# Performance work log

Hardware: AMD Instinct MI355X
Metric: run time of the kernel (lower is better)

Reference implementation:

```python
import jax, jax.numpy as jnp
import numpy as np

RES = 32
SPATIAL = 3
NUM_VOCAB = 3
EMBED_DIM = 256
BATCH = 8
LAYER_SIZES = (8, 64, 512, 4096, 32768)   # full-octree token counts at depths 1..5
CONV_SIZE = {3: 4, 4: 8}                  # layer_idx -> conv kernel==stride (2**(sd-1), 2**sd)
PARAM_NAMES = ([f"val_emb_{l}" for l in range(5)] + [f"pos_emb_{l}" for l in range(5)]
               + [f"dep_emb_{l}" for l in range(3)]
               + ["conv_w_3", "conv_b_3", "conv_w_4", "conv_b_4"])


def _forward(value, depth, position, params):
    # depth layout is static per construction: tokens sorted by depth with LAYER_SIZES counts,
    # so the per-depth boolean masking of the torch code reduces to static slices.
    outs, start = [], 0
    for l, n in enumerate(LAYER_SIZES):
        v = value[:, start:start + n]          # [B, n]
        d = depth[:, start:start + n]          # [B, n]
        p = position[:, start:start + n]       # [B, n, SPATIAL]
        start += n
        pe = params[f"pos_emb_{l}"]            # [SPATIAL, 2*RES, E]
        x = (params[f"val_emb_{l}"][v]
             + pe[0][p[..., 0]] + pe[1][p[..., 1]] + pe[2][p[..., 2]])
        if l < 3:
            # BasicEmbeddingA: value + depth + spatial embeddings summed
            x = x + params[f"dep_emb_{l}"][d]
        else:
            # ConvolutionEmbeddingA: Conv1d(E, E, kernel=stride=k) shrinks seq by k.
            # stride==kernel -> expressible as a reshape + einsum contraction.
            k = CONV_SIZE[l]
            B, T, E = x.shape
            xr = x.reshape(B, T // k, k, E)
            x = jnp.einsum('btke,oek->bto', xr, params[f"conv_w_{l}"]) + params[f"conv_b_{l}"]
        outs.append(x)
    # all samples have identical per-depth lengths -> pad_sequence is a plain concat
    return jnp.concatenate(outs, axis=1)       # [B, 5704, E]


def setup_inputs() -> dict:
    keys = iter(jax.random.split(jax.random.key(0), 64))
    S = sum(LAYER_SIZES)
    value = jax.random.randint(next(keys), (BATCH, S), 1, NUM_VOCAB + 1, dtype=jnp.int32)
    depth = jnp.broadcast_to(
        jnp.concatenate([jnp.full((n,), l + 1, jnp.int32) for l, n in enumerate(LAYER_SIZES)]),
        (BATCH, S))
    position = jax.random.randint(next(keys), (BATCH, S, SPATIAL), 1, 2 * RES, dtype=jnp.int32)
    inp = {"value": value, "depth": depth, "position": position}

    def emb(k, n):  # padding_idx=0 -> zero row
        return (jax.random.normal(k, (n, EMBED_DIM)) * 0.02).at[0].set(0.0)

    for l in range(5):
        inp[f"val_emb_{l}"] = emb(next(keys), NUM_VOCAB + 1)
        inp[f"pos_emb_{l}"] = (jax.random.normal(next(keys), (SPATIAL, 2 * RES, EMBED_DIM)) * 0.02).at[:, 0].set(0.0)
    for l in range(3):
        inp[f"dep_emb_{l}"] = emb(next(keys), 6)
    for l in (3, 4):
        k = CONV_SIZE[l]
        inp[f"conv_w_{l}"] = jax.random.normal(next(keys), (EMBED_DIM, EMBED_DIM, k)) / np.float32(np.sqrt(EMBED_DIM * k))
        inp[f"conv_b_{l}"] = jnp.zeros((EMBED_DIM,), jnp.float32)
    return inp


def reference(value, depth, position,
              val_emb_0, val_emb_1, val_emb_2, val_emb_3, val_emb_4,
              pos_emb_0, pos_emb_1, pos_emb_2, pos_emb_3, pos_emb_4,
              dep_emb_0, dep_emb_1, dep_emb_2,
              conv_w_3, conv_b_3, conv_w_4, conv_b_4):
    params = dict(zip(PARAM_NAMES, (val_emb_0, val_emb_1, val_emb_2, val_emb_3, val_emb_4,
                                    pos_emb_0, pos_emb_1, pos_emb_2, pos_emb_3, pos_emb_4,
                                    dep_emb_0, dep_emb_1, dep_emb_2,
                                    conv_w_3, conv_b_3, conv_w_4, conv_b_4)))
    return _forward(value, depth, position, params)
```

## Files before the change

### kernel.cpp

```cpp
#include <hip/hip_runtime.h>

#define S_TOT 37448
#define OUT_T 5704
#define EMB 256
#define TROWS 384
#define TSZ (TROWS * 256)

typedef unsigned short u16;
typedef __bf16 bf16x8 __attribute__((ext_vector_type(8)));
typedef float f32x4 __attribute__((ext_vector_type(4)));
typedef float f32x2 __attribute__((ext_vector_type(2)));
typedef unsigned short u16x4 __attribute__((ext_vector_type(4)));
typedef unsigned short u16x8 __attribute__((ext_vector_type(8)));

__device__ __forceinline__ u16 f2bf(float f) {
  union { float f; unsigned int i; } v;
  v.f = f;
  unsigned int x = v.i;
  return (u16)((x + 0x7fffu + ((x >> 16) & 1u)) >> 16);
}
__device__ __forceinline__ f32x2 bfp(unsigned u) {
  union { unsigned u; float f; } lo, hi;
  lo.u = u << 16;
  hi.u = u & 0xffff0000u;
  return (f32x2){lo.f, hi.f};
}

#define GLOAD_LDS16(g, l)                                                     \
  __builtin_amdgcn_global_load_lds((const __attribute__((address_space(1))) void*)(g), \
                                   (__attribute__((address_space(3))) void*)(l), 16, 0, 0)

__global__ __launch_bounds__(256) void transpose_w(
    const float* __restrict__ w3, const float* __restrict__ w4,
    u16* __restrict__ wt3, u16* __restrict__ wt4) {
  const int i = blockIdx.x * 256 + threadIdx.x;
  if (i < 256 * 1024) {
    const int o = i >> 10, c = i & 1023, kk = c >> 8, e = c & 255;
    wt3[i] = f2bf(w3[o * 1024 + e * 4 + kk]);
  }
  if (i < 256 * 2048) {
    const int o = i >> 11, c = i & 2047, kk = c >> 8, e = c & 255;
    wt4[i] = f2bf(w4[o * 2048 + e * 8 + kk]);
  }
}

__global__ __launch_bounds__(512) void proj_tables(
    const float* __restrict__ ve3, const float* __restrict__ pe3, const u16* __restrict__ wt3,
    const float* __restrict__ ve4, const float* __restrict__ pe4, const u16* __restrict__ wt4,
    u16* __restrict__ Tm) {
  __shared__ __align__(16) u16 As[64 * 32];
  __shared__ __align__(16) u16 Bs[256 * 32];
  const int bid = blockIdx.x;
  const int p = bid / 6, rb = bid % 6;
  const float *ve, *pe;
  const u16* wt;
  int K, kk;
  if (p < 4) { ve = ve3; pe = pe3; wt = wt3; K = 1024; kk = p; }
  else       { ve = ve4; pe = pe4; wt = wt4; K = 2048; kk = p - 4; }
  u16* To = Tm + (long)p * TSZ;
  const int tid = threadIdx.x;
  const int lane = tid & 63, wid = tid >> 6;
  const int wr = wid >> 2, wc = wid & 3;
  const int fr = lane & 15, fq = lane >> 4;
  const int row0 = rb * 64;

  const int arow = tid >> 3, acg = tid & 7;
  const int agran = acg >> 1, ahalf = acg & 1;
  const int aoff = arow * 32 + (agran ^ ((arow >> 1) & 3)) * 8 + ahalf * 4;
  const int gr = row0 + arow;
  const bool two = (gr < 256);
  const float* s1 = two ? (ve + (gr >> 6) * 256) : (pe + (gr - 192) * 256);
  const float* s2 = two ? (pe + (gr & 63) * 256) : nullptr;

  f32x4 acc[2][4];
#pragma unroll
  for (int m = 0; m < 2; ++m)
#pragma unroll
    for (int n = 0; n < 4; ++n) acc[m][n] = (f32x4){0.f, 0.f, 0.f, 0.f};

  for (int s = 0; s < 8; ++s) {
    {
      float4 x = *(const float4*)(s1 + s * 32 + acg * 4);
      if (two) {
        const float4 y = *(const float4*)(s2 + s * 32 + acg * 4);
        x.x += y.x; x.y += y.y; x.z += y.z; x.w += y.w;
      }
      u16x4 pk;
      pk[0] = f2bf(x.x); pk[1] = f2bf(x.y); pk[2] = f2bf(x.z); pk[3] = f2bf(x.w);
      *(u16x4*)(&As[aoff]) = pk;
    }
#pragma unroll
    for (int j = 0; j < 2; ++j) {
      const int rl = j * 128 + wid * 16 + (lane >> 2);
      const int gc = (lane & 3) ^ ((rl >> 1) & 3);
      const u16* src = wt + (long)rl * K + (kk * 8 + s) * 32 + gc * 8;
      u16* dst = &Bs[(j * 128 + wid * 16) * 32];
      GLOAD_LDS16(src, dst);
    }
    __syncthreads();
    bf16x8 af[2], bfv[4];
#pragma unroll
    for (int m = 0; m < 2; ++m) {
      const int r = wr * 32 + m * 16 + fr;
      u16x8 t = *(const u16x8*)(&As[r * 32 + (fq ^ ((r >> 1) & 3)) * 8]);
      af[m] = __builtin_bit_cast(bf16x8, t);
    }
#pragma unroll
    for (int n = 0; n < 4; ++n) {
      const int o = wc * 64 + n * 16 + fr;
      u16x8 t = *(const u16x8*)(&Bs[o * 32 + (fq ^ ((o >> 1) & 3)) * 8]);
      bfv[n] = __builtin_bit_cast(bf16x8, t);
    }
#pragma unroll
    for (int m = 0; m < 2; ++m)
#pragma unroll
      for (int n = 0; n < 4; ++n)
        acc[m][n] = __builtin_amdgcn_mfma_f32_16x16x32_bf16(af[m], bfv[n], acc[m][n], 0, 0, 0);
    __syncthreads();
  }
#pragma unroll
  for (int m = 0; m < 2; ++m)
#pragma unroll
    for (int reg = 0; reg < 4; ++reg) {
      const int r = row0 + wr * 32 + m * 16 + fq * 4 + reg;
#pragma unroll
      for (int n = 0; n < 4; ++n)
        To[r * 256 + wc * 64 + n * 16 + fr] = f2bf(acc[m][n][reg]);
    }
}

template <int CK, int LOG2T, int S0, int OUT0>
__device__ __forceinline__ void rowpair_gather(
    int pair, int lane, const int* __restrict__ value,
    const int* __restrict__ position, const u16* __restrict__ Tp,
    const float4& bz0, const float4& bz1, float* __restrict__ out) {
  constexpr int T = 1 << LOG2T;
  const int row = pair * 2 + (lane >> 5);
  const int l32 = lane & 31;
  const int b = row >> LOG2T, to = row & (T - 1);
  const long base = (long)b * S_TOT + S0 + to * CK;
  int vv[CK];
  *(int4*)vv = *(const int4*)(value + base);
  if constexpr (CK == 8) *(int4*)(vv + 4) = *(const int4*)(value + base + 4);
  int pp[3 * CK];
#pragma unroll
  for (int j = 0; j < 3 * CK / 2; ++j)
    *(int2*)(pp + 2 * j) = *(const int2*)(position + base * 3 + 2 * j);

  const int o0 = l32 * 8;
  f32x2 ac0 = (f32x2){bz0.x, bz0.y};
  f32x2 ac1 = (f32x2){bz0.z, bz0.w};
  f32x2 ac2 = (f32x2){bz1.x, bz1.y};
  f32x2 ac3 = (f32x2){bz1.z, bz1.w};

  uint4 A[CK][3];
#pragma unroll
  for (int kk = 0; kk < CK; ++kk) {
    const u16* tb = Tp + kk * TSZ;
    A[kk][0] = *(const uint4*)(tb + ((vv[kk] << 6) | pp[3 * kk + 0]) * 256 + o0);
    A[kk][1] = *(const uint4*)(tb + (256 + pp[3 * kk + 1]) * 256 + o0);
    A[kk][2] = *(const uint4*)(tb + (320 + pp[3 * kk + 2]) * 256 + o0);
  }
#pragma unroll
  for (int kk = 0; kk < CK; ++kk) {
#pragma unroll
    for (int t = 0; t < 3; ++t) {
      ac0 += bfp(A[kk][t].x);
      ac1 += bfp(A[kk][t].y);
      ac2 += bfp(A[kk][t].z);
      ac3 += bfp(A[kk][t].w);
    }
  }
  float* op = out + ((long)b * OUT_T + OUT0 + to) * 256 + o0;
  const f32x4 r0 = (f32x4){ac0[0], ac0[1], ac1[0], ac1[1]};
  const f32x4 r1 = (f32x4){ac2[0], ac2[1], ac3[0], ac3[1]};
  __builtin_nontemporal_store(r0, (f32x4*)op);
  __builtin_nontemporal_store(r1, (f32x4*)(op + 4));
}

__global__ __launch_bounds__(256) void fused_main(
    const int* __restrict__ value, const int* __restrict__ depth,
    const int* __restrict__ position,
    const u16* __restrict__ Tm3, const float* __restrict__ b3,
    const u16* __restrict__ Tm4, const float* __restrict__ b4,
    const float* __restrict__ ve0, const float* __restrict__ pe0, const float* __restrict__ de0,
    const float* __restrict__ ve1, const float* __restrict__ pe1, const float* __restrict__ de1,
    const float* __restrict__ ve2, const float* __restrict__ pe2, const float* __restrict__ de2,
    float* __restrict__ out) {
  const int wid = threadIdx.x >> 6, lane = threadIdx.x & 63;
  const int bid = blockIdx.x;
  const int o0 = (lane & 31) * 8;
  if (bid < 2048) {
    const int pair0 = (bid * 4 + wid) * 2;
    const float4 bz0 = *(const float4*)(b4 + o0);
    const float4 bz1 = *(const float4*)(b4 + o0 + 4);
#pragma unroll
    for (int pr = 0; pr < 2; ++pr)
      rowpair_gather<8, 12, 4680, 1608>(pair0 + pr, lane, value, position, Tm4,
                                        bz0, bz1, out);
  } else if (bid < 2560) {
    const int pair0 = ((bid - 2048) * 4 + wid) * 2;
    const float4 bz0 = *(const float4*)(b3 + o0);
    const float4 bz1 = *(const float4*)(b3 + o0 + 4);
#pragma unroll
    for (int pr = 0; pr < 2; ++pr)
      rowpair_gather<4, 10, 584, 584>(pair0 + pr, lane, value, position, Tm3,
                                      bz0, bz1, out);
  } else {
    const int tok0 = ((bid - 2560) * 4 + wid) * 4;
    const int e = lane * 4;
#pragma unroll
    for (int rr = 0; rr < 4; ++rr) {
      const int tok = tok0 + rr;
      const int b = tok / 584;
      const int t = tok - b * 584;
      const float *ve, *pe, *de;
      if (t < 8)       { ve = ve0; pe = pe0; de = de0; }
      else if (t < 72) { ve = ve1; pe = pe1; de = de1; }
      else             { ve = ve2; pe = pe2; de = de2; }
      const long base = (long)b * S_TOT + t;
      const int v = value[base];
      const int d = depth[base];
      const int p0 = position[base * 3 + 0];
      const int p1 = position[base * 3 + 1];
      const int p2 = position[base * 3 + 2];
      const float4 x = *(const float4*)(ve + v * EMB + e);
      const float4 y = *(const float4*)(pe + p0 * EMB + e);
      const float4 z = *(const float4*)(pe + (64 + p1) * EMB + e);
      const float4 u = *(const float4*)(pe + (128 + p2) * EMB + e);
      const float4 w = *(const float4*)(de + d * EMB + e);
      f32x4 r;
      r[0] = x.x + y.x + z.x + u.x + w.x;
      r[1] = x.y + y.y + z.y + u.y + w.y;
      r[2] = x.z + y.z + z.z + u.z + w.z;
      r[3] = x.w + y.w + z.w + u.w + w.w;
      __builtin_nontemporal_store(r, (f32x4*)(out + ((long)b * OUT_T + t) * EMB + e));
    }
  }
}

__global__ __launch_bounds__(256) void emb_small(
    const int* __restrict__ value, const int* __restrict__ depth,
    const int* __restrict__ position,
    const float* __restrict__ ve0, const float* __restrict__ pe0, const float* __restrict__ de0,
    const float* __restrict__ ve1, const float* __restrict__ pe1, const float* __restrict__ de1,
    const float* __restrict__ ve2, const float* __restrict__ pe2, const float* __restrict__ de2,
    float* __restrict__ out) {
  const int tok = blockIdx.x * 4 + (threadIdx.x >> 6);
  const int lane = threadIdx.x & 63;
  const int b = tok / 584;
  const int t = tok - b * 584;
  const float *ve, *pe, *de;
  if (t < 8)       { ve = ve0; pe = pe0; de = de0; }
  else if (t < 72) { ve = ve1; pe = pe1; de = de1; }
  else             { ve = ve2; pe = pe2; de = de2; }
  const long base = (long)b * S_TOT + t;
  const int v = value[base];
  const int d = depth[base];
  const int p0 = position[base * 3 + 0];
  const int p1 = position[base * 3 + 1];
  const int p2 = position[base * 3 + 2];
  const int e = lane * 4;
  const float4 x = *(const float4*)(ve + v * EMB + e);
  const float4 y = *(const float4*)(pe + p0 * EMB + e);
  const float4 z = *(const float4*)(pe + (64 + p1) * EMB + e);
  const float4 u = *(const float4*)(pe + (128 + p2) * EMB + e);
  const float4 w = *(const float4*)(de + d * EMB + e);
  float4 r;
  r.x = x.x + y.x + z.x + u.x + w.x;
  r.y = x.y + y.y + z.y + u.y + w.y;
  r.z = x.z + y.z + z.z + u.z + w.z;
  r.w = x.w + y.w + z.w + u.w + w.w;
  *(float4*)(out + ((long)b * OUT_T + t) * EMB + e) = r;
}

template <int K, int LOG2T, int CK, int S0, int OUT0>
__device__ __forceinline__ void conv_tile(
    int bid, const int* __restrict__ value, const int* __restrict__ position,
    const float* __restrict__ ve, const float* __restrict__ pe,
    const float* __restrict__ wraw, const float* __restrict__ bias,
    float* __restrict__ out,
    u16 (*As)[64 * 32], u16 (*Bs)[256 * 32], unsigned* idxc) {
  constexpr int T = 1 << LOG2T;
  constexpr int NS = K / 32;
  const int tid = threadIdx.x;
  const int lane = tid & 63;
  const int wid = tid >> 6;
  const int wr = wid >> 2;
  const int wc = wid & 3;
  const int fr = lane & 15;
  const int fq = lane >> 4;
  const int row0 = bid * 64;
  for (int e = tid; e < 64 * CK; e += 512) {
    const int r = e / CK, kk = e % CK;
    const int grow = row0 + r;
    const int b = grow >> LOG2T;
    const int to = grow & (T - 1);
    const long sidx = (long)b * S_TOT + (S0 + to * CK + kk);
    const int* pp = position + sidx * 3;
    idxc[e] = (unsigned)value[sidx] | ((unsigned)pp[0] << 8) |
              ((unsigned)pp[1] << 16) | ((unsigned)pp[2] << 24);
  }
  __syncthreads();
  const int arow = tid >> 3;
  const int acg = tid & 7;
  const int agran = acg >> 1, ahalf = acg & 1;
  const int aoff = arow * 32 + (agran ^ ((arow >> 1) & 3)) * 8 + ahalf * 4;
  auto gatherA = [&](int s, float4& r) {
    const int kk = s >> 3;
    const int e0 = (s & 7) * 32 + acg * 4;
    const unsigned q = idxc[arow * CK + kk];
    const int v = q & 255, p0 = (q >> 8) & 255, p1 = (q >> 16) & 255, p2 = q >> 24;
    float4 x = *(const float4*)(ve + v * EMB + e0);
    float4 y = *(const float4*)(pe + p0 * EMB + e0);
    float4 z = *(const float4*)(pe + (64 + p1) * EMB + e0);
    float4 u = *(const float4*)(pe + (128 + p2) * EMB + e0);
    r.x = x.x + y.x + z.x + u.x;
    r.y = x.y + y.y + z.y + u.y;
    r.z = x.z + y.z + z.z + u.z;
    r.w = x.w + y.w + z.w + u.w;
  };
  auto writeA = [&](int buf, const float4& r) {
    u16x4 p;
    p[0] = f2bf(r.x); p[1] = f2bf(r.y); p[2] = f2bf(r.z); p[3] = f2bf(r.w);
    *(u16x4*)(&As[buf][aoff]) = p;
  };
  auto issueB = [&](int s, int buf) {
    const int o = tid >> 1;
    const int hr = tid & 1;
    const int kk = s >> 3, e0 = (s & 7) * 32;
    const int osw = (o >> 1) & 3;
#pragma unroll
    for (int g2 = 0; g2 < 2; ++g2) {
      const int g = hr * 2 + g2;
      u16x8 r;
#pragma unroll
      for (int c = 0; c < 8; ++c)
        r[c] = f2bf(wraw[(long)o * (EMB * CK) + (e0 + g * 8 + c) * CK + kk]);
      *(u16x8*)(&Bs[buf][o * 32 + (g ^ osw) * 8]) = r;
    }
  };
  f32x4 acc[2][4];
#pragma unroll
  for (int m = 0; m < 2; ++m)
#pragma unroll
    for (int n = 0; n < 4; ++n) acc[m][n] = (f32x4){0.f, 0.f, 0.f, 0.f};
  {
    float4 a0;
    gatherA(0, a0);
    issueB(0, 0);
    writeA(0, a0);
  }
  __syncthreads();
  int cur = 0;
  for (int s = 0; s < NS; ++s) {
    const int nxt = cur ^ 1;
    const bool more = (s + 1 < NS);
    float4 pa;
    if (more) {
      gatherA(s + 1, pa);
      issueB(s + 1, nxt);
    }
    bf16x8 af[2], bfv[4];
#pragma unroll
    for (int m = 0; m < 2; ++m) {
      const int r = wr * 32 + m * 16 + fr;
      u16x8 t = *(const u16x8*)(&As[cur][r * 32 + (fq ^ ((r >> 1) & 3)) * 8]);
      af[m] = __builtin_bit_cast(bf16x8, t);
    }
#pragma unroll
    for (int n = 0; n < 4; ++n) {
      const int o = wc * 64 + n * 16 + fr;
      u16x8 t = *(const u16x8*)(&Bs[cur][o * 32 + (fq ^ ((o >> 1) & 3)) * 8]);
      bfv[n] = __builtin_bit_cast(bf16x8, t);
    }
#pragma unroll
    for (int m = 0; m < 2; ++m)
#pragma unroll
      for (int n = 0; n < 4; ++n)
        acc[m][n] = __builtin_amdgcn_mfma_f32_16x16x32_bf16(af[m], bfv[n], acc[m][n], 0, 0, 0);
    if (more) writeA(nxt, pa);
    __syncthreads();
    cur = nxt;
  }
  float bz[4];
#pragma unroll
  for (int n = 0; n < 4; ++n) bz[n] = bias[wc * 64 + n * 16 + fr];
#pragma unroll
  for (int m = 0; m < 2; ++m) {
#pragma unroll
    for (int reg = 0; reg < 4; ++reg) {
      const int grow = row0 + wr * 32 + m * 16 + fq * 4 + reg;
      const int bb = grow >> LOG2T;
      const int to = grow & (T - 1);
      float* op = out + ((long)bb * OUT_T + OUT0 + to) * EMB + wc * 64 + fr;
#pragma unroll
      for (int n = 0; n < 4; ++n) op[n * 16] = acc[m][n][reg] + bz[n];
    }
  }
}

__global__ __launch_bounds__(512, 4) void conv_fused(
    const int* __restrict__ value, const int* __restrict__ position,
    const float* __restrict__ ve3, const float* __restrict__ pe3,
    const float* __restrict__ w3, const float* __restrict__ b3,
    const float* __restrict__ ve4, const float* __restrict__ pe4,
    const float* __restrict__ w4, const float* __restrict__ b4,
    float* __restrict__ out) {
  __shared__ __align__(16) u16 As[2][64 * 32];
  __shared__ __align__(16) u16 Bs[2][256 * 32];
  __shared__ __align__(16) unsigned idxc[64 * 8];
  const int g = blockIdx.x / 5, r = blockIdx.x % 5;
  if (r == 0)
    conv_tile<1024, 10, 4, 584, 584>(g, value, position, ve3, pe3, w3, b3,
                                     out, As, Bs, idxc);
  else
    conv_tile<2048, 12, 8, 4680, 1608>(g * 4 + (r - 1), value, position, ve4,
                                       pe4, w4, b4, out, As, Bs, idxc);
}

extern "C" void kernel_launch(void* const* d_in, const int* in_sizes, int n_in,
                              void* d_out, int out_size, void* d_ws, size_t ws_size,
                              hipStream_t stream) {
  const int* value = (const int*)d_in[0];
  const int* depth = (const int*)d_in[1];
  const int* position = (const int*)d_in[2];
  const float* ve0 = (const float*)d_in[3];
  const float* pe0 = (const float*)d_in[4];
  const float* ve1 = (const float*)d_in[5];
  const float* pe1 = (const float*)d_in[6];
  const float* ve2 = (const float*)d_in[7];
  const float* pe2 = (const float*)d_in[8];
  const float* ve3 = (const float*)d_in[9];
  const float* pe3 = (const float*)d_in[10];
  const float* ve4 = (const float*)d_in[11];
  const float* pe4 = (const float*)d_in[12];
  const float* de0 = (const float*)d_in[13];
  const float* de1 = (const float*)d_in[14];
  const float* de2 = (const float*)d_in[15];
  const float* w3 = (const float*)d_in[16];
  const float* b3 = (const float*)d_in[17];
  const float* w4 = (const float*)d_in[18];
  const float* b4 = (const float*)d_in[19];
  float* out = (float*)d_out;

  u16* wt3 = (u16*)d_ws;
  u16* wt4 = wt3 + 256 * 1024;
  u16* Tm = wt4 + 256 * 2048;
  const size_t need = (size_t)(256 * 1024 + 256 * 2048 + 12 * TSZ) * sizeof(u16);

  if (ws_size >= need) {
    transpose_w<<<(256 * 2048) / 256, 256, 0, stream>>>(w3, w4, wt3, wt4);
    proj_tables<<<72, 512, 0, stream>>>(ve3, pe3, wt3, ve4, pe4, wt4, Tm);
    fused_main<<<2852, 256, 0, stream>>>(value, depth, position,
                                         Tm, b3, Tm + 4 * TSZ, b4,
                                         ve0, pe0, de0, ve1, pe1, de1,
                                         ve2, pe2, de2, out);
  } else {
    emb_small<<<1168, 256, 0, stream>>>(value, depth, position, ve0, pe0, de0,
                                        ve1, pe1, de1, ve2, pe2, de2, out);
    conv_fused<<<640, 512, 0, stream>>>(value, position, ve3, pe3, w3, b3,
                                        ve4, pe4, w4, b4, out);
  }
}
```

Before: 44.68 us.

## Split proj_tables output columns across blocks and batch two rows' gathers together

proj_tables now splits each 64-row tile's 256 output columns across two 256-thread blocks, launching 144 blocks instead of 72 so more CUs work on the table projection. The A-tile staging is reworked so each thread writes 8 bf16 values. In fused_main, each wave now issues all table gathers for two row-pairs before doing any accumulation, which gives more memory loads in flight. The cost is higher register pressure from holding twice as many gathered vectors.

Measured after the change: 44.56 us, median of 2. About the same (-0.3%).

```diff
diff --git a/kernel.cpp b/kernel.cpp
--- a/kernel.cpp
+++ b/kernel.cpp
@@ -44,14 +44,16 @@
   }
 }
 
-__global__ __launch_bounds__(512) void proj_tables(
+__global__ __launch_bounds__(256) void proj_tables(
     const float* __restrict__ ve3, const float* __restrict__ pe3, const u16* __restrict__ wt3,
     const float* __restrict__ ve4, const float* __restrict__ pe4, const u16* __restrict__ wt4,
     u16* __restrict__ Tm) {
   __shared__ __align__(16) u16 As[64 * 32];
-  __shared__ __align__(16) u16 Bs[256 * 32];
+  __shared__ __align__(16) u16 Bs[128 * 32];
   const int bid = blockIdx.x;
-  const int p = bid / 6, rb = bid % 6;
+  const int p = bid / 12;
+  const int rcb = bid % 12;
+  const int rb = rcb >> 1, cb = rcb & 1;
   const float *ve, *pe;
   const u16* wt;
   int K, kk;
@@ -60,13 +62,12 @@
   u16* To = Tm + (long)p * TSZ;
   const int tid = threadIdx.x;
   const int lane = tid & 63, wid = tid >> 6;
-  const int wr = wid >> 2, wc = wid & 3;
+  const int wr = wid >> 1, wc = wid & 1;
   const int fr = lane & 15, fq = lane >> 4;
   const int row0 = rb * 64;
 
-  const int arow = tid >> 3, acg = tid & 7;
-  const int agran = acg >> 1, ahalf = acg & 1;
-  const int aoff = arow * 32 + (agran ^ ((arow >> 1) & 3)) * 8 + ahalf * 4;
+  const int arow = tid >> 2, acg = tid & 3;
+  const int aoff = arow * 32 + (acg ^ ((arow >> 1) & 3)) * 8;
   const int gr = row0 + arow;
   const bool two = (gr < 256);
   const float* s1 = two ? (ve + (gr >> 6) * 256) : (pe + (gr - 192) * 256);
@@ -80,21 +81,25 @@
 
   for (int s = 0; s < 8; ++s) {
     {
-      float4 x = *(const float4*)(s1 + s * 32 + acg * 4);
+      float4 x0 = *(const float4*)(s1 + s * 32 + acg * 8);
+      float4 x1 = *(const float4*)(s1 + s * 32 + acg * 8 + 4);
       if (two) {
-        const float4 y = *(const float4*)(s2 + s * 32 + acg * 4);
-        x.x += y.x; x.y += y.y; x.z += y.z; x.w += y.w;
+        const float4 y0 = *(const float4*)(s2 + s * 32 + acg * 8);
+        const float4 y1 = *(const float4*)(s2 + s * 32 + acg * 8 + 4);
+        x0.x += y0.x; x0.y += y0.y; x0.z += y0.z; x0.w += y0.w;
+        x1.x += y1.x; x1.y += y1.y; x1.z += y1.z; x1.w += y1.w;
       }
-      u16x4 pk;
-      pk[0] = f2bf(x.x); pk[1] = f2bf(x.y); pk[2] = f2bf(x.z); pk[3] = f2bf(x.w);
-      *(u16x4*)(&As[aoff]) = pk;
+      u16x8 pk;
+      pk[0] = f2bf(x0.x); pk[1] = f2bf(x0.y); pk[2] = f2bf(x0.z); pk[3] = f2bf(x0.w);
+      pk[4] = f2bf(x1.x); pk[5] = f2bf(x1.y); pk[6] = f2bf(x1.z); pk[7] = f2bf(x1.w);
+      *(u16x8*)(&As[aoff]) = pk;
     }
 #pragma unroll
     for (int j = 0; j < 2; ++j) {
-      const int rl = j * 128 + wid * 16 + (lane >> 2);
-      const int gc = (lane & 3) ^ ((rl >> 1) & 3);
-      const u16* src = wt + (long)rl * K + (kk * 8 + s) * 32 + gc * 8;
-      u16* dst = &Bs[(j * 128 + wid * 16) * 32];
+      const int rloc = j * 64 + wid * 16 + (lane >> 2);
+      const int gc = (lane & 3) ^ ((rloc >> 1) & 3);
+      const u16* src = wt + (long)(cb * 128 + rloc) * K + (kk * 8 + s) * 32 + gc * 8;
+      u16* dst = &Bs[(j * 64 + wid * 16) * 32];
       GLOAD_LDS16(src, dst);
     }
     __syncthreads();
@@ -125,57 +130,95 @@
       const int r = row0 + wr * 32 + m * 16 + fq * 4 + reg;
 #pragma unroll
       for (int n = 0; n < 4; ++n)
-        To[r * 256 + wc * 64 + n * 16 + fr] = f2bf(acc[m][n][reg]);
+        To[r * 256 + cb * 128 + wc * 64 + n * 16 + fr] = f2bf(acc[m][n][reg]);
     }
 }
 
 template <int CK, int LOG2T, int S0, int OUT0>
-__device__ __forceinline__ void rowpair_gather(
-    int pair, int lane, const int* __restrict__ value,
+__device__ __forceinline__ void rowquad_gather(
+    int pair0, int lane, const int* __restrict__ value,
     const int* __restrict__ position, const u16* __restrict__ Tp,
     const float4& bz0, const float4& bz1, float* __restrict__ out) {
   constexpr int T = 1 << LOG2T;
-  const int row = pair * 2 + (lane >> 5);
   const int l32 = lane & 31;
-  const int b = row >> LOG2T, to = row & (T - 1);
-  const long base = (long)b * S_TOT + S0 + to * CK;
-  int vv[CK];
-  *(int4*)vv = *(const int4*)(value + base);
-  if constexpr (CK == 8) *(int4*)(vv + 4) = *(const int4*)(value + base + 4);
-  int pp[3 * CK];
-#pragma unroll
-  for (int j = 0; j < 3 * CK / 2; ++j)
-    *(int2*)(pp + 2 * j) = *(const int2*)(position + base * 3 + 2 * j);
-
   const int o0 = l32 * 8;
-  f32x2 ac0 = (f32x2){bz0.x, bz0.y};
-  f32x2 ac1 = (f32x2){bz0.z, bz0.w};
-  f32x2 ac2 = (f32x2){bz1.x, bz1.y};
-  f32x2 ac3 = (f32x2){bz1.z, bz1.w};
-
-  uint4 A[CK][3];
+  const int rowA = pair0 * 2 + (lane >> 5);
+  const int rowB = rowA + 2;
+
+  const int bA = rowA >> LOG2T, toA = rowA & (T - 1);
+  const int bB = rowB >> LOG2T, toB = rowB & (T - 1);
+  const long baseA = (long)bA * S_TOT + S0 + toA * CK;
+  const long baseB = (long)bB * S_TOT + S0 + toB * CK;
+  int vvA[CK], vvB[CK];
+  *(int4*)vvA = *(const int4*)(value + baseA);
+  *(int4*)vvB = *(const int4*)(value + baseB);
+  if constexpr (CK == 8) {
+    *(int4*)(vvA + 4) = *(const int4*)(value + baseA + 4);
+    *(int4*)(vvB + 4) = *(const int4*)(value + baseB + 4);
+  }
+  int ppA[3 * CK], ppB[3 * CK];
+#pragma unroll
+  for (int j = 0; j < 3 * CK / 2; ++j) {
+    *(int2*)(ppA + 2 * j) = *(const int2*)(position + baseA * 3 + 2 * j);
+    *(int2*)(ppB + 2 * j) = *(const int2*)(position + baseB * 3 + 2 * j);
+  }
+
+  uint4 A[CK][3], B[CK][3];
 #pragma unroll
   for (int kk = 0; kk < CK; ++kk) {
     const u16* tb = Tp + kk * TSZ;
-    A[kk][0] = *(const uint4*)(tb + ((vv[kk] << 6) | pp[3 * kk + 0]) * 256 + o0);
-    A[kk][1] = *(const uint4*)(tb + (256 + pp[3 * kk + 1]) * 256 + o0);
-    A[kk][2] = *(const uint4*)(tb + (320 + pp[3 * kk + 2]) * 256 + o0);
+    A[kk][0] = *(const uint4*)(tb + ((vvA[kk] << 6) | ppA[3 * kk + 0]) * 256 + o0);
+    A[kk][1] = *(const uint4*)(tb + (256 + ppA[3 * kk + 1]) * 256 + o0);
+    A[kk][2] = *(const uint4*)(tb + (320 + ppA[3 * kk + 2]) * 256 + o0);
   }
 #pragma unroll
   for (int kk = 0; kk < CK; ++kk) {
-#pragma unroll
-    for (int t = 0; t < 3; ++t) {
-      ac0 += bfp(A[kk][t].x);
-      ac1 += bfp(A[kk][t].y);
-      ac2 += bfp(A[kk][t].z);
-      ac3 += bfp(A[kk][t].w);
-    }
-  }
-  float* op = out + ((long)b * OUT_T + OUT0 + to) * 256 + o0;
-  const f32x4 r0 = (f32x4){ac0[0], ac0[1], ac1[0], ac1[1]};
-  const f32x4 r1 = (f32x4){ac2[0], ac2[1], ac3[0], ac3[1]};
-  __builtin_nontemporal_store(r0, (f32x4*)op);
-  __builtin_nontemporal_store(r1, (f32x4*)(op + 4));
+    const u16* tb = Tp + kk * TSZ;
+    B[kk][0] = *(const uint4*)(tb + ((vvB[kk] << 6) | ppB[3 * kk + 0]) * 256 + o0);
+    B[kk][1] = *(const uint4*)(tb + (256 + ppB[3 * kk + 1]) * 256 + o0);
+    B[kk][2] = *(const uint4*)(tb + (320 + ppB[3 * kk + 2]) * 256 + o0);
+  }
+
+  {
+    f32x2 ac0 = (f32x2){bz0.x, bz0.y};
+    f32x2 ac1 = (f32x2){bz0.z, bz0.w};
+    f32x2 ac2 = (f32x2){bz1.x, bz1.y};
+    f32x2 ac3 = (f32x2){bz1.z, bz1.w};
+#pragma unroll
+    for (int kk = 0; kk < CK; ++kk)
+#pragma unroll
+      for (int t = 0; t < 3; ++t) {
+        ac0 += bfp(A[kk][t].x);
+        ac1 += bfp(A[kk][t].y);
+        ac2 += bfp(A[kk][t].z);
+        ac3 += bfp(A[kk][t].w);
+      }
+    float* op = out + ((long)bA * OUT_T + OUT0 + toA) * 256 + o0;
+    const f32x4 r0 = (f32x4){ac0[0], ac0[1], ac1[0], ac1[1]};
+    const f32x4 r1 = (f32x4){ac2[0], ac2[1], ac3[0], ac3[1]};
+    __builtin_nontemporal_store(r0, (f32x4*)op);
+    __builtin_nontemporal_store(r1, (f32x4*)(op + 4));
+  }
+  {
+    f32x2 ac0 = (f32x2){bz0.x, bz0.y};
+    f32x2 ac1 = (f32x2){bz0.z, bz0.w};
+    f32x2 ac2 = (f32x2){bz1.x, bz1.y};
+    f32x2 ac3 = (f32x2){bz1.z, bz1.w};
+#pragma unroll
+    for (int kk = 0; kk < CK; ++kk)
+#pragma unroll
+      for (int t = 0; t < 3; ++t) {
+        ac0 += bfp(B[kk][t].x);
+        ac1 += bfp(B[kk][t].y);
+        ac2 += bfp(B[kk][t].z);
+        ac3 += bfp(B[kk][t].w);
+      }
+    float* op = out + ((long)bB * OUT_T + OUT0 + toB) * 256 + o0;
+    const f32x4 r0 = (f32x4){ac0[0], ac0[1], ac1[0], ac1[1]};
+    const f32x4 r1 = (f32x4){ac2[0], ac2[1], ac3[0], ac3[1]};
+    __builtin_nontemporal_store(r0, (f32x4*)op);
+    __builtin_nontemporal_store(r1, (f32x4*)(op + 4));
+  }
 }
 
 __global__ __launch_bounds__(256) void fused_main(
@@ -194,18 +237,14 @@
     const int pair0 = (bid * 4 + wid) * 2;
     const float4 bz0 = *(const float4*)(b4 + o0);
     const float4 bz1 = *(const float4*)(b4 + o0 + 4);
-#pragma unroll
-    for (int pr = 0; pr < 2; ++pr)
-      rowpair_gather<8, 12, 4680, 1608>(pair0 + pr, lane, value, position, Tm4,
-                                        bz0, bz1, out);
+    rowquad_gather<8, 12, 4680, 1608>(pair0, lane, value, position, Tm4,
+                                      bz0, bz1, out);
   } else if (bid < 2560) {
     const int pair0 = ((bid - 2048) * 4 + wid) * 2;
     const float4 bz0 = *(const float4*)(b3 + o0);
     const float4 bz1 = *(const float4*)(b3 + o0 + 4);
-#pragma unroll
-    for (int pr = 0; pr < 2; ++pr)
-      rowpair_gather<4, 10, 584, 584>(pair0 + pr, lane, value, position, Tm3,
-                                      bz0, bz1, out);
+    rowquad_gather<4, 10, 584, 584>(pair0, lane, value, position, Tm3,
+                                    bz0, bz1, out);
   } else {
     const int tok0 = ((bid - 2560) * 4 + wid) * 4;
     const int e = lane * 4;
@@ -451,7 +490,7 @@
 
   if (ws_size >= need) {
     transpose_w<<<(256 * 2048) / 256, 256, 0, stream>>>(w3, w4, wt3, wt4);
-    proj_tables<<<72, 512, 0, stream>>>(ve3, pe3, wt3, ve4, pe4, wt4, Tm);
+    proj_tables<<<144, 256, 0, stream>>>(ve3, pe3, wt3, ve4, pe4, wt4, Tm);
     fused_main<<<2852, 256, 0, stream>>>(value, depth, position,
                                          Tm, b3, Tm + 4 * TSZ, b4,
                                          ve0, pe0, de0, ve1, pe1, de1,
```
